# Optimization experiments

Hardware: AMD Instinct MI355X
Metric: run time of the kernel (lower is better)

The kernel has to match this reference:

```python
import jax, jax.numpy as jnp
import numpy as np

N, E = 30000, 180000
IN, H, OUT = 3000, 512, 30


def _segment_softmax(e, dst, n):
    # numerically stable softmax over incoming edges of each destination node
    m = jax.ops.segment_max(e, dst, num_segments=n)
    m = jnp.where(jnp.isfinite(m), m, 0.0)  # nodes with no in-edges
    ex = jnp.exp(e - m[dst])
    den = jax.ops.segment_sum(ex, dst, num_segments=n)
    return ex / den[dst]


def _gat(x, src, dst, Ws, Wd, a_s, a_d, n, alpha=None):
    """edGATConv (heads=1, no self-loops, no bias).
    xs = lin_s(x); attention score from lin_s(x)[src] and lin_d(x)[dst];
    out[i] = sum_{e: dst_e=i} alpha_e * xs[src_e].
    If alpha is given (tie_alpha), reuse it instead of recomputing."""
    xs = x @ Ws.T  # [n, F_out]
    if alpha is None:
        xd = x @ Wd.T
        e = jax.nn.leaky_relu(xs[src] @ a_s + xd[dst] @ a_d, 0.2)  # [E]
        alpha = _segment_softmax(e, dst, n)
    out = jax.ops.segment_sum(alpha[:, None] * xs[src], dst, num_segments=n)
    return out, alpha


def setup_inputs() -> dict:
    key = jax.random.key(0)
    ks = jax.random.split(key, 7)
    features = jax.random.normal(ks[0], (N, IN), dtype=jnp.float32)
    edge_index = jax.random.randint(ks[1], (2, E), 0, N)
    W1s = jax.random.normal(ks[2], (H, IN), dtype=jnp.float32) * 0.02
    W1d = jax.random.normal(ks[3], (H, IN), dtype=jnp.float32) * 0.02
    a1s = jax.random.normal(ks[4], (H,), dtype=jnp.float32) * 0.1
    a1d = jax.random.normal(ks[5], (H,), dtype=jnp.float32) * 0.1
    W2s = jax.random.normal(ks[6], (OUT, H), dtype=jnp.float32) * 0.05
    return {"features": features, "edge_index": edge_index,
            "W1s": W1s, "W1d": W1d, "a1s": a1s, "a1d": a1d, "W2s": W2s}


def reference(features, edge_index, W1s, W1d, a1s, a1d, W2s):
    src, dst = edge_index[0], edge_index[1]
    n = features.shape[0]
    # conv1: attentive GAT layer, stores tie_alpha
    h1, alpha1 = _gat(features, src, dst, W1s, W1d, a1s, a1d, n)
    h1 = jax.nn.elu(h1)
    # conv2: aslinear=True -> plain linear with lin_s
    h2 = h1 @ W2s.T  # [N, OUT]
    # conv3: weights tied to conv2 transposed, alpha tied to conv1
    # W3s = W2s.T so xs3 = h2 @ W3s.T = h2 @ W2s
    h3, _ = _gat(h2, src, dst, W2s.T, None, None, None, n, alpha=alpha1)
    h3 = jax.nn.elu(h3)
    # conv4: aslinear, weight tied to conv1 transposed: h3 @ W4s.T = h3 @ W1s
    h4 = h3 @ W1s  # [N, IN]
    return (h2, h4)
```

## Files before the change

kernel.cpp:

```cpp
#include <hip/hip_runtime.h>

typedef unsigned short u16;
typedef __bf16 bf16_t;
typedef bf16_t bf16x8 __attribute__((ext_vector_type(8)));
typedef float f32x4 __attribute__((ext_vector_type(4)));
typedef u16 u16x8 __attribute__((ext_vector_type(8)));

#define AS1 __attribute__((address_space(1)))
#define AS3 __attribute__((address_space(3)))

__device__ __forceinline__ u16 f2bf(float f) {
    union { float f; unsigned u; } v; v.f = f;
    unsigned r = v.u + 0x7FFFu + ((v.u >> 16) & 1u);
    return (u16)(r >> 16);
}
__device__ __forceinline__ float bf2f(u16 s) {
    union { unsigned u; float f; } v; v.u = ((unsigned)s) << 16;
    return v.f;
}

__device__ __forceinline__ void gload_lds16(const u16* g, u16* l) {
    __builtin_amdgcn_global_load_lds((AS1 const void*)g, (AS3 void*)l, 16, 0, 0);
}

template <bool OUT_BF16, bool GUARD>
__global__ __launch_bounds__(256) void gemm_bt(
    const u16* __restrict__ A, const u16* __restrict__ B, void* __restrict__ Cv,
    int K, int ldc, int Mreal, int Nreal)
{
    __shared__ u16 As[128 * 64];
    __shared__ u16 Bs[128 * 64];
    const int t = threadIdx.x;
    const int w = t >> 6, l = t & 63;

    const int nwg = gridDim.x * gridDim.y;
    const int lin = blockIdx.y * gridDim.x + blockIdx.x;
    const int xcd = lin & 7, loc = lin >> 3;
    const int q = nwg >> 3, r = nwg & 7;
    const int swz = (xcd < r ? xcd * (q + 1) : r * (q + 1) + (xcd - r) * q) + loc;
    const int bx = swz % gridDim.x, by = swz / gridDim.x;

    const int m0 = by * 128, n0 = bx * 128;
    const int wm = (w >> 1) * 64, wn = (w & 1) * 64;

    const int srow = w << 5;
    const int lrow = l >> 3, lc = l & 7;

    f32x4 acc[4][4] = {};

    for (int kt = 0; kt < K; kt += 64) {
#pragma unroll
        for (int i = 0; i < 4; ++i) {
            int row = srow + i * 8 + lrow;
            int gc = ((lc ^ (row & 7)) << 3);
            const u16* ga = A + (size_t)(m0 + row) * K + kt + gc;
            const u16* gb = B + (size_t)(n0 + row) * K + kt + gc;
            u16* la = &As[(srow + i * 8) * 64];
            u16* lb = &Bs[(srow + i * 8) * 64];
            gload_lds16(ga, la);
            gload_lds16(gb, lb);
        }
        asm volatile("s_waitcnt vmcnt(0)");
        __syncthreads();

#pragma unroll
        for (int kk = 0; kk < 2; ++kk) {
            bf16x8 af[4], bfr[4];
            int kc = kk * 4 + (l >> 4);
#pragma unroll
            for (int mi = 0; mi < 4; ++mi) {
                int row = wm + mi * 16 + (l & 15);
                af[mi] = *(const bf16x8*)&As[row * 64 + ((kc ^ (row & 7)) << 3)];
            }
#pragma unroll
            for (int ni = 0; ni < 4; ++ni) {
                int col = wn + ni * 16 + (l & 15);
                bfr[ni] = *(const bf16x8*)&Bs[col * 64 + ((kc ^ (col & 7)) << 3)];
            }
#pragma unroll
            for (int mi = 0; mi < 4; ++mi)
#pragma unroll
                for (int ni = 0; ni < 4; ++ni)
                    acc[mi][ni] = __builtin_amdgcn_mfma_f32_16x16x32_bf16(
                        af[mi], bfr[ni], acc[mi][ni], 0, 0, 0);
        }
        __syncthreads();
    }

#pragma unroll
    for (int mi = 0; mi < 4; ++mi) {
#pragma unroll
        for (int qq = 0; qq < 4; ++qq) {
            int row = m0 + wm + mi * 16 + (l >> 4) * 4 + qq;
            if (GUARD && row >= Mreal) continue;
#pragma unroll
            for (int ni = 0; ni < 4; ++ni) {
                int col = n0 + wn + ni * 16 + (l & 15);
                if (GUARD && col >= Nreal) continue;
                float v = acc[mi][ni][qq];
                if (OUT_BF16) ((u16*)Cv)[(size_t)row * ldc + col] = f2bf(v);
                else          ((float*)Cv)[(size_t)row * ldc + col] = v;
            }
        }
    }
}

__global__ void k_vd(const float* __restrict__ W1d, const float* __restrict__ a1d,
                     float* __restrict__ vd) {
    int i = blockIdx.x * 256 + threadIdx.x;
    if (i >= 3000) return;
    float acc = 0.f;
    for (int h = 0; h < 512; ++h) acc += W1d[(size_t)h * 3000 + i] * a1d[h];
    vd[i] = acc;
}

__global__ void k_w1sb(const float* __restrict__ W1s, u16* __restrict__ wb) {
    int idx = blockIdx.x * 256 + threadIdx.x;
    if (idx >= 512 * 768) return;
    int n = idx / 768, g = idx % 768, k = g * 4;
    ushort4 o = make_ushort4(0, 0, 0, 0);
    if (k < 3000) {
        float4 v = *(const float4*)(W1s + (size_t)n * 3000 + k);
        o.x = f2bf(v.x); o.y = f2bf(v.y); o.z = f2bf(v.z); o.w = f2bf(v.w);
    }
    *(ushort4*)(wb + (size_t)n * 3072 + k) = o;
}

__global__ void k_w1st(const float* __restrict__ W1s, u16* __restrict__ wt) {
    int idx = blockIdx.x * 256 + threadIdx.x;
    if (idx >= 3072 * 512) return;
    int n = idx >> 9, k = idx & 511;
    wt[idx] = (n < 3000) ? f2bf(W1s[(size_t)k * 3000 + n]) : (u16)0;
}

__global__ void k_w2b(const float* __restrict__ W2s, u16* __restrict__ wb) {
    int idx = blockIdx.x * 256 + threadIdx.x;
    if (idx >= 128 * 512) return;
    int n = idx >> 9, k = idx & 511;
    wb[idx] = (n < 30) ? f2bf(W2s[(size_t)n * 512 + k]) : (u16)0;
}

__global__ void k_convX(const float* __restrict__ X, u16* __restrict__ xb,
                        const float* __restrict__ vd, float* __restrict__ sd) {
    __shared__ float red[4];
    int n = blockIdx.x, t = threadIdx.x;
    u16* brow = xb + (size_t)n * 3072;
    if (n < 30000) {
        const float* xrow = X + (size_t)n * 3000;
        float part = 0.f;
#pragma unroll
        for (int it = 0; it < 3; ++it) {
            int c = (t + it * 256) * 4;
            ushort4 o = make_ushort4(0, 0, 0, 0);
            if (c < 3000) {
                float4 v = *(const float4*)(xrow + c);
                float4 wv = *(const float4*)(vd + c);
                o.x = f2bf(v.x); o.y = f2bf(v.y); o.z = f2bf(v.z); o.w = f2bf(v.w);
                part += v.x * wv.x + v.y * wv.y + v.z * wv.z + v.w * wv.w;
            }
            *(ushort4*)(brow + c) = o;
        }
#pragma unroll
        for (int s = 32; s; s >>= 1) part += __shfl_xor(part, s);
        if ((t & 63) == 0) red[t >> 6] = part;
        __syncthreads();
        if (t == 0) sd[n] = red[0] + red[1] + red[2] + red[3];
    } else {
#pragma unroll
        for (int it = 0; it < 3; ++it)
            *(ushort4*)(brow + (t + it * 256) * 4) = make_ushort4(0, 0, 0, 0);
    }
}

__global__ void k_ss(const u16* __restrict__ xs1, const float* __restrict__ a1s,
                     float* __restrict__ ss) {
    int w = threadIdx.x >> 6, l = threadIdx.x & 63;
    int n = blockIdx.x * 4 + w;
    if (n >= 30000) return;
    const u16* row = xs1 + (size_t)n * 512 + l * 8;
    const float* a = a1s + l * 8;
    ushort4 u0 = *(const ushort4*)row;
    ushort4 u1 = *(const ushort4*)(row + 4);
    float4 w0 = *(const float4*)a;
    float4 w1 = *(const float4*)(a + 4);
    float acc = bf2f(u0.x) * w0.x + bf2f(u0.y) * w0.y + bf2f(u0.z) * w0.z + bf2f(u0.w) * w0.w
              + bf2f(u1.x) * w1.x + bf2f(u1.y) * w1.y + bf2f(u1.z) * w1.z + bf2f(u1.w) * w1.w;
#pragma unroll
    for (int s = 32; s; s >>= 1) acc += __shfl_xor(acc, s);
    if (l == 0) ss[n] = acc;
}

__global__ void k_deg(const int* __restrict__ dst, unsigned* __restrict__ deg) {
    int j = blockIdx.x * 256 + threadIdx.x;
    if (j < 180000) atomicAdd(&deg[dst[j]], 1u);
}

__global__ void k_scan1(const unsigned* __restrict__ deg, unsigned* __restrict__ bsum, int n) {
    __shared__ unsigned ws[4];
    int i = blockIdx.x * 256 + threadIdx.x;
    unsigned v = (i < n) ? deg[i] : 0u;
#pragma unroll
    for (int s = 32; s; s >>= 1) v += __shfl_xor(v, s);
    if ((threadIdx.x & 63) == 0) ws[threadIdx.x >> 6] = v;
    __syncthreads();
    if (threadIdx.x == 0) bsum[blockIdx.x] = ws[0] + ws[1] + ws[2] + ws[3];
}

__global__ void k_scan2(const unsigned* __restrict__ bsum, unsigned* __restrict__ boff,
                        unsigned* __restrict__ off_end, int nb) {
    __shared__ unsigned tmp[128];
    int t = threadIdx.x;
    unsigned v = (t < nb) ? bsum[t] : 0u;
    tmp[t] = v;
    __syncthreads();
    for (int s = 1; s < 128; s <<= 1) {
        unsigned a = (t >= s) ? tmp[t - s] : 0u;
        __syncthreads();
        tmp[t] += a;
        __syncthreads();
    }
    if (t < nb) boff[t] = tmp[t] - v;
    if (t == nb - 1) *off_end = tmp[t];
}

__global__ void k_scan3(const unsigned* __restrict__ deg, const unsigned* __restrict__ boff,
                        unsigned* __restrict__ off, unsigned* __restrict__ cur, int n) {
    __shared__ unsigned tmp[256];
    int b = blockIdx.x, t = threadIdx.x, i = b * 256 + t;
    unsigned v = (i < n) ? deg[i] : 0u;
    tmp[t] = v;
    __syncthreads();
    for (int s = 1; s < 256; s <<= 1) {
        unsigned a = (t >= s) ? tmp[t - s] : 0u;
        __syncthreads();
        tmp[t] += a;
        __syncthreads();
    }
    if (i < n) {
        unsigned o = boff[b] + tmp[t] - v;
        off[i] = o;
        cur[i] = o;
    }
}

__global__ void k_fill(const int* __restrict__ dst, unsigned* __restrict__ cur,
                       unsigned* __restrict__ csr) {
    int j = blockIdx.x * 256 + threadIdx.x;
    if (j >= 180000) return;
    unsigned pos = atomicAdd(&cur[dst[j]], 1u);
    csr[pos] = (unsigned)j;
}

__global__ void k_soft(const int* __restrict__ src, const float* __restrict__ ss,
                       const float* __restrict__ sd, float* __restrict__ alpha,
                       const unsigned* __restrict__ csr, const unsigned* __restrict__ off) {
    int t = threadIdx.x;
    int g = t >> 3, l = t & 7;
    int n = blockIdx.x * 32 + g;
    if (n >= 30000) return;
    unsigned lo = off[n], hi = off[n + 1];
    if (lo == hi) return;
    float sdn = sd[n];
    float m = -1e30f;
    for (unsigned i = lo + l; i < hi; i += 8) {
        float v = ss[src[csr[i]]] + sdn;
        v = v > 0.f ? v : 0.2f * v;
        m = fmaxf(m, v);
    }
    m = fmaxf(m, __shfl_xor(m, 1));
    m = fmaxf(m, __shfl_xor(m, 2));
    m = fmaxf(m, __shfl_xor(m, 4));
    float den = 0.f;
    for (unsigned i = lo + l; i < hi; i += 8) {
        float v = ss[src[csr[i]]] + sdn;
        v = v > 0.f ? v : 0.2f * v;
        den += expf(v - m);
    }
    den += __shfl_xor(den, 1);
    den += __shfl_xor(den, 2);
    den += __shfl_xor(den, 4);
    float inv = 1.f / den;
    for (unsigned i = lo + l; i < hi; i += 8) {
        unsigned j = csr[i];
        float v = ss[src[j]] + sdn;
        v = v > 0.f ? v : 0.2f * v;
        alpha[j] = expf(v - m) * inv;
    }
}

__global__ void k_agg(const u16* __restrict__ xin, const float* __restrict__ alpha,
                      const unsigned* __restrict__ csr, const unsigned* __restrict__ off,
                      const int* __restrict__ src, u16* __restrict__ outb, int nvalid) {
    int w = threadIdx.x >> 6, l = threadIdx.x & 63;
    int n = blockIdx.x * 4 + w;
    float acc[8] = {};
    if (n < nvalid) {
        unsigned lo = off[n], hi = off[n + 1];
        for (unsigned i = lo; i < hi; ++i) {
            unsigned j = csr[i];
            float av = alpha[j];
            int sj = src[j];
            u16x8 row = *(const u16x8*)&xin[(size_t)sj * 512 + l * 8];
#pragma unroll
            for (int k = 0; k < 8; ++k) acc[k] += av * bf2f(row[k]);
        }
    }
    u16x8 o;
#pragma unroll
    for (int k = 0; k < 8; ++k) {
        float a = acc[k] > 0.f ? acc[k] : expf(acc[k]) - 1.f;
        o[k] = f2bf(a);
    }
    *(u16x8*)&outb[(size_t)n * 512 + l * 8] = o;
}

__global__ void k_xs3(const float* __restrict__ h2, const float* __restrict__ W2s,
                      u16* __restrict__ xs3) {
    int t = threadIdx.x;
    size_t n0 = (size_t)blockIdx.x * 8;
    float w0[30], w1[30];
#pragma unroll
    for (int o = 0; o < 30; ++o) {
        w0[o] = W2s[(size_t)o * 512 + t];
        w1[o] = W2s[(size_t)o * 512 + t + 256];
    }
    for (int r = 0; r < 8; ++r) {
        size_t n = n0 + r;
        const float* hr = h2 + n * 30;
        float a0 = 0.f, a1 = 0.f;
#pragma unroll
        for (int o = 0; o < 30; ++o) {
            float v = hr[o];
            a0 += v * w0[o];
            a1 += v * w1[o];
        }
        xs3[n * 512 + t] = f2bf(a0);
        xs3[n * 512 + t + 256] = f2bf(a1);
    }
}

extern "C" void kernel_launch(void* const* d_in, const int* in_sizes, int n_in,
                              void* d_out, int out_size, void* d_ws, size_t ws_size,
                              hipStream_t stream) {
    const float* X   = (const float*)d_in[0];
    const int*   ei  = (const int*)d_in[1];
    const float* W1s = (const float*)d_in[2];
    const float* W1d = (const float*)d_in[3];
    const float* a1s = (const float*)d_in[4];
    const float* a1d = (const float*)d_in[5];
    const float* W2s = (const float*)d_in[6];
    const int* src = ei;
    const int* dst = ei + 180000;

    float* out = (float*)d_out;
    float* h2 = out;
    float* h4 = out + 900000;

    char* ob = (char*)(out + 900000);
    u16* xbf  = (u16*)ob;
    u16* xs1b = (u16*)(ob + 184811520);
    u16* h1b  = (u16*)(ob + 184811520 + 30801920);
    u16* xs3b = (u16*)(ob + 184811520 + 30801920 + 30801920);

    char* w = (char*)d_ws;
    auto carve = [&](size_t bytes) { char* p = w; w += (bytes + 255) & ~(size_t)255; return p; };
    u16* w1sb = (u16*)carve((size_t)512 * 3072 * 2);
    u16* w1st = (u16*)carve((size_t)3072 * 512 * 2);
    u16* w2sb = (u16*)carve((size_t)128 * 512 * 2);
    u16* h3b  = (u16*)carve((size_t)30080 * 512 * 2);
    float* vd    = (float*)carve(3000 * 4);
    float* ss    = (float*)carve(30000 * 4);
    float* sd    = (float*)carve(30000 * 4);
    float* alpha = (float*)carve(180000 * 4);
    unsigned* deg = (unsigned*)carve(30000 * 4);
    unsigned* off = (unsigned*)carve(30004 * 4);
    unsigned* cur = (unsigned*)carve(30000 * 4);
    unsigned* csr = (unsigned*)carve(180000 * 4);
    unsigned* bsum = (unsigned*)carve(128 * 4);
    unsigned* boff = (unsigned*)carve(128 * 4);

    hipMemsetAsync(deg, 0, 30000 * 4, stream);

    k_vd  <<<12, 256, 0, stream>>>(W1d, a1d, vd);
    k_w1sb<<<1536, 256, 0, stream>>>(W1s, w1sb);
    k_w1st<<<6144, 256, 0, stream>>>(W1s, w1st);
    k_w2b <<<256, 256, 0, stream>>>(W2s, w2sb);
    k_convX<<<30080, 256, 0, stream>>>(X, xbf, vd, sd);

    gemm_bt<true, false><<<dim3(4, 235), 256, 0, stream>>>(xbf, w1sb, xs1b, 3072, 512, 0, 0);

    k_ss  <<<7500, 256, 0, stream>>>(xs1b, a1s, ss);
    k_deg <<<704, 256, 0, stream>>>(dst, deg);
    k_scan1<<<118, 256, 0, stream>>>(deg, bsum, 30000);
    k_scan2<<<1, 128, 0, stream>>>(bsum, boff, &off[30000], 118);
    k_scan3<<<118, 256, 0, stream>>>(deg, boff, off, cur, 30000);
    k_fill<<<704, 256, 0, stream>>>(dst, cur, csr);
    k_soft<<<938, 256, 0, stream>>>(src, ss, sd, alpha, csr, off);

    k_agg <<<7520, 256, 0, stream>>>(xs1b, alpha, csr, off, src, h1b, 30000);

    gemm_bt<false, true><<<dim3(1, 235), 256, 0, stream>>>(h1b, w2sb, h2, 512, 30, 30000, 30);

    k_xs3 <<<3750, 256, 0, stream>>>(h2, W2s, xs3b);
    k_agg <<<7520, 256, 0, stream>>>(xs3b, alpha, csr, off, src, h3b, 30000);

    gemm_bt<false, true><<<dim3(24, 235), 256, 0, stream>>>(h3b, w1st, h4, 512, 3000, 30000, 3000);
}
```

Baseline: 711.5 us.

## Fold attention source score into input pass and fuse h2/xs3 GEMMs

The source attention score ss is now computed as X·(W1s^T a1s) inside the input-conversion pass, which removes the separate k_ss kernel over xs1. The W2s^T W2s product is precomputed into a combined weight matrix, so one GEMM over h1 writes both h2 and xs3 and the k_xs3 kernel goes away. The W1s transpose kernel is also rewritten to go through an LDS tile for coalesced access. In exchange, the combined GEMM does about five times the N-width of the old h2 GEMM, and ss now comes from fp32 X instead of bf16 xs1, which changes rounding slightly.

```diff
diff --git a/kernel.cpp b/kernel.cpp
--- a/kernel.cpp
+++ b/kernel.cpp
@@ -105,13 +105,95 @@
     }
 }
 
+__global__ __launch_bounds__(256) void gemm_combo(
+    const u16* __restrict__ A, const u16* __restrict__ B,
+    float* __restrict__ h2, u16* __restrict__ xs3)
+{
+    __shared__ u16 As[128 * 64];
+    __shared__ u16 Bs[128 * 64];
+    const int t = threadIdx.x;
+    const int w = t >> 6, l = t & 63;
+
+    const int nwg = gridDim.x * gridDim.y;
+    const int lin = blockIdx.y * gridDim.x + blockIdx.x;
+    const int xcd = lin & 7, loc = lin >> 3;
+    const int q = nwg >> 3, r = nwg & 7;
+    const int swz = (xcd < r ? xcd * (q + 1) : r * (q + 1) + (xcd - r) * q) + loc;
+    const int bx = swz % gridDim.x, by = swz / gridDim.x;
+
+    const int m0 = by * 128, n0 = bx * 128;
+    const int wm = (w >> 1) * 64, wn = (w & 1) * 64;
+    const int srow = w << 5;
+    const int lrow = l >> 3, lc = l & 7;
+
+    f32x4 acc[4][4] = {};
+
+    for (int kt = 0; kt < 512; kt += 64) {
+#pragma unroll
+        for (int i = 0; i < 4; ++i) {
+            int row = srow + i * 8 + lrow;
+            int gc = ((lc ^ (row & 7)) << 3);
+            gload_lds16(A + (size_t)(m0 + row) * 512 + kt + gc, &As[(srow + i * 8) * 64]);
+            gload_lds16(B + (size_t)(n0 + row) * 512 + kt + gc, &Bs[(srow + i * 8) * 64]);
+        }
+        asm volatile("s_waitcnt vmcnt(0)");
+        __syncthreads();
+
+#pragma unroll
+        for (int kk = 0; kk < 2; ++kk) {
+            bf16x8 af[4], bfr[4];
+            int kc = kk * 4 + (l >> 4);
+#pragma unroll
+            for (int mi = 0; mi < 4; ++mi) {
+                int row = wm + mi * 16 + (l & 15);
+                af[mi] = *(const bf16x8*)&As[row * 64 + ((kc ^ (row & 7)) << 3)];
+            }
+#pragma unroll
+            for (int ni = 0; ni < 4; ++ni) {
+                int col = wn + ni * 16 + (l & 15);
+                bfr[ni] = *(const bf16x8*)&Bs[col * 64 + ((kc ^ (col & 7)) << 3)];
+            }
+#pragma unroll
+            for (int mi = 0; mi < 4; ++mi)
+#pragma unroll
+                for (int ni = 0; ni < 4; ++ni)
+                    acc[mi][ni] = __builtin_amdgcn_mfma_f32_16x16x32_bf16(
+                        af[mi], bfr[ni], acc[mi][ni], 0, 0, 0);
+        }
+        __syncthreads();
+    }
+
+#pragma unroll
+    for (int mi = 0; mi < 4; ++mi) {
+#pragma unroll
+        for (int qq = 0; qq < 4; ++qq) {
+            int row = m0 + wm + mi * 16 + (l >> 4) * 4 + qq;
+#pragma unroll
+            for (int ni = 0; ni < 4; ++ni) {
+                int col = n0 + wn + ni * 16 + (l & 15);
+                float v = acc[mi][ni][qq];
+                if (col < 30) {
+                    if (row < 30000) h2[(size_t)row * 30 + col] = v;
+                } else if (col >= 128) {
+                    xs3[(size_t)row * 512 + (col - 128)] = f2bf(v);
+                }
+            }
+        }
+    }
+}
+
 __global__ void k_vd(const float* __restrict__ W1d, const float* __restrict__ a1d,
-                     float* __restrict__ vd) {
+                     const float* __restrict__ W1s, const float* __restrict__ a1s,
+                     float* __restrict__ vd, float* __restrict__ vs) {
     int i = blockIdx.x * 256 + threadIdx.x;
     if (i >= 3000) return;
-    float acc = 0.f;
-    for (int h = 0; h < 512; ++h) acc += W1d[(size_t)h * 3000 + i] * a1d[h];
-    vd[i] = acc;
+    float ad = 0.f, as = 0.f;
+    for (int h = 0; h < 512; ++h) {
+        ad += W1d[(size_t)h * 3000 + i] * a1d[h];
+        as += W1s[(size_t)h * 3000 + i] * a1s[h];
+    }
+    vd[i] = ad;
+    vs[i] = as;
 }
 
 __global__ void k_w1sb(const float* __restrict__ W1s, u16* __restrict__ wb) {
@@ -127,67 +209,79 @@
 }
 
 __global__ void k_w1st(const float* __restrict__ W1s, u16* __restrict__ wt) {
+    __shared__ float tile[64][65];
+    int t = threadIdx.x;
+    int i0 = blockIdx.x * 64;
+    int h0 = blockIdx.y * 64;
+    int il = t & 63, hq = t >> 6;
+#pragma unroll
+    for (int rr = 0; rr < 16; ++rr) {
+        int hl = rr * 4 + hq;
+        int i = i0 + il;
+        tile[hl][il] = (i < 3000) ? W1s[(size_t)(h0 + hl) * 3000 + i] : 0.f;
+    }
+    __syncthreads();
+#pragma unroll
+    for (int rr = 0; rr < 16; ++rr) {
+        int il2 = rr * 4 + hq;
+        wt[(size_t)(i0 + il2) * 512 + h0 + il] = f2bf(tile[il][il2]);
+    }
+}
+
+__global__ void k_wcomb(const float* __restrict__ W2s, u16* __restrict__ wb) {
     int idx = blockIdx.x * 256 + threadIdx.x;
-    if (idx >= 3072 * 512) return;
+    if (idx >= 640 * 512) return;
     int n = idx >> 9, k = idx & 511;
-    wt[idx] = (n < 3000) ? f2bf(W1s[(size_t)k * 3000 + n]) : (u16)0;
-}
-
-__global__ void k_w2b(const float* __restrict__ W2s, u16* __restrict__ wb) {
-    int idx = blockIdx.x * 256 + threadIdx.x;
-    if (idx >= 128 * 512) return;
-    int n = idx >> 9, k = idx & 511;
-    wb[idx] = (n < 30) ? f2bf(W2s[(size_t)n * 512 + k]) : (u16)0;
+    float v = 0.f;
+    if (n < 30) {
+        v = W2s[(size_t)n * 512 + k];
+    } else if (n >= 128) {
+        int i = n - 128;
+        for (int o = 0; o < 30; ++o)
+            v += W2s[(size_t)o * 512 + i] * W2s[(size_t)o * 512 + k];
+    }
+    wb[idx] = f2bf(v);
 }
 
 __global__ void k_convX(const float* __restrict__ X, u16* __restrict__ xb,
-                        const float* __restrict__ vd, float* __restrict__ sd) {
-    __shared__ float red[4];
+                        const float* __restrict__ vd, const float* __restrict__ vs,
+                        float* __restrict__ sd, float* __restrict__ ss) {
+    __shared__ float redd[4], reds[4];
     int n = blockIdx.x, t = threadIdx.x;
     u16* brow = xb + (size_t)n * 3072;
     if (n < 30000) {
         const float* xrow = X + (size_t)n * 3000;
-        float part = 0.f;
+        float pd = 0.f, ps = 0.f;
 #pragma unroll
         for (int it = 0; it < 3; ++it) {
             int c = (t + it * 256) * 4;
             ushort4 o = make_ushort4(0, 0, 0, 0);
             if (c < 3000) {
                 float4 v = *(const float4*)(xrow + c);
-                float4 wv = *(const float4*)(vd + c);
+                float4 wd = *(const float4*)(vd + c);
+                float4 ws = *(const float4*)(vs + c);
                 o.x = f2bf(v.x); o.y = f2bf(v.y); o.z = f2bf(v.z); o.w = f2bf(v.w);
-                part += v.x * wv.x + v.y * wv.y + v.z * wv.z + v.w * wv.w;
+                pd += v.x * wd.x + v.y * wd.y + v.z * wd.z + v.w * wd.w;
+                ps += v.x * ws.x + v.y * ws.y + v.z * ws.z + v.w * ws.w;
             }
             *(ushort4*)(brow + c) = o;
         }
 #pragma unroll
-        for (int s = 32; s; s >>= 1) part += __shfl_xor(part, s);
-        if ((t & 63) == 0) red[t >> 6] = part;
-        __syncthreads();
-        if (t == 0) sd[n] = red[0] + red[1] + red[2] + red[3];
+        for (int s = 32; s; s >>= 1) {
+            pd += __shfl_xor(pd, s);
+            ps += __shfl_xor(ps, s);
+        }
+        if ((t & 63) == 0) { redd[t >> 6] = pd; reds[t >> 6] = ps; }
+        __syncthreads();
+        if (t == 0) {
+            sd[n] = redd[0] + redd[1] + redd[2] + redd[3];
+            ss[n] = reds[0] + reds[1] + reds[2] + reds[3];
+        }
     } else {
 #pragma unroll
         for (int it = 0; it < 3; ++it)
             *(ushort4*)(brow + (t + it * 256) * 4) = make_ushort4(0, 0, 0, 0);
     }
-}
-
-__global__ void k_ss(const u16* __restrict__ xs1, const float* __restrict__ a1s,
-                     float* __restrict__ ss) {
-    int w = threadIdx.x >> 6, l = threadIdx.x & 63;
-    int n = blockIdx.x * 4 + w;
-    if (n >= 30000) return;
-    const u16* row = xs1 + (size_t)n * 512 + l * 8;
-    const float* a = a1s + l * 8;
-    ushort4 u0 = *(const ushort4*)row;
-    ushort4 u1 = *(const ushort4*)(row + 4);
-    float4 w0 = *(const float4*)a;
-    float4 w1 = *(const float4*)(a + 4);
-    float acc = bf2f(u0.x) * w0.x + bf2f(u0.y) * w0.y + bf2f(u0.z) * w0.z + bf2f(u0.w) * w0.w
-              + bf2f(u1.x) * w1.x + bf2f(u1.y) * w1.y + bf2f(u1.z) * w1.z + bf2f(u1.w) * w1.w;
-#pragma unroll
-    for (int s = 32; s; s >>= 1) acc += __shfl_xor(acc, s);
-    if (l == 0) ss[n] = acc;
 }
 
 __global__ void k_deg(const int* __restrict__ dst, unsigned* __restrict__ deg) {
@@ -314,31 +408,6 @@
     *(u16x8*)&outb[(size_t)n * 512 + l * 8] = o;
 }
 
-__global__ void k_xs3(const float* __restrict__ h2, const float* __restrict__ W2s,
-                      u16* __restrict__ xs3) {
-    int t = threadIdx.x;
-    size_t n0 = (size_t)blockIdx.x * 8;
-    float w0[30], w1[30];
-#pragma unroll
-    for (int o = 0; o < 30; ++o) {
-        w0[o] = W2s[(size_t)o * 512 + t];
-        w1[o] = W2s[(size_t)o * 512 + t + 256];
-    }
-    for (int r = 0; r < 8; ++r) {
-        size_t n = n0 + r;
-        const float* hr = h2 + n * 30;
-        float a0 = 0.f, a1 = 0.f;
-#pragma unroll
-        for (int o = 0; o < 30; ++o) {
-            float v = hr[o];
-            a0 += v * w0[o];
-            a1 += v * w1[o];
-        }
-        xs3[n * 512 + t] = f2bf(a0);
-        xs3[n * 512 + t + 256] = f2bf(a1);
-    }
-}
-
 extern "C" void kernel_launch(void* const* d_in, const int* in_sizes, int n_in,
                               void* d_out, int out_size, void* d_ws, size_t ws_size,
                               hipStream_t stream) {
@@ -364,11 +433,12 @@
 
     char* w = (char*)d_ws;
     auto carve = [&](size_t bytes) { char* p = w; w += (bytes + 255) & ~(size_t)255; return p; };
-    u16* w1sb = (u16*)carve((size_t)512 * 3072 * 2);
-    u16* w1st = (u16*)carve((size_t)3072 * 512 * 2);
-    u16* w2sb = (u16*)carve((size_t)128 * 512 * 2);
-    u16* h3b  = (u16*)carve((size_t)30080 * 512 * 2);
-    float* vd    = (float*)carve(3000 * 4);
+    u16* w1sb  = (u16*)carve((size_t)512 * 3072 * 2);
+    u16* w1st  = (u16*)carve((size_t)3072 * 512 * 2);
+    u16* wcomb = (u16*)carve((size_t)640 * 512 * 2);
+    u16* h3b   = (u16*)carve((size_t)30080 * 512 * 2);
+    float* vd    = (float*)carve(3008 * 4);
+    float* vs    = (float*)carve(3008 * 4);
     float* ss    = (float*)carve(30000 * 4);
     float* sd    = (float*)carve(30000 * 4);
     float* alpha = (float*)carve(180000 * 4);
@@ -381,15 +451,14 @@
 
     hipMemsetAsync(deg, 0, 30000 * 4, stream);
 
-    k_vd  <<<12, 256, 0, stream>>>(W1d, a1d, vd);
-    k_w1sb<<<1536, 256, 0, stream>>>(W1s, w1sb);
-    k_w1st<<<6144, 256, 0, stream>>>(W1s, w1st);
-    k_w2b <<<256, 256, 0, stream>>>(W2s, w2sb);
-    k_convX<<<30080, 256, 0, stream>>>(X, xbf, vd, sd);
+    k_vd   <<<12, 256, 0, stream>>>(W1d, a1d, W1s, a1s, vd, vs);
+    k_w1sb <<<1536, 256, 0, stream>>>(W1s, w1sb);
+    k_w1st <<<dim3(48, 8), 256, 0, stream>>>(W1s, w1st);
+    k_wcomb<<<1280, 256, 0, stream>>>(W2s, wcomb);
+    k_convX<<<30080, 256, 0, stream>>>(X, xbf, vd, vs, sd, ss);
 
     gemm_bt<true, false><<<dim3(4, 235), 256, 0, stream>>>(xbf, w1sb, xs1b, 3072, 512, 0, 0);
 
-    k_ss  <<<7500, 256, 0, stream>>>(xs1b, a1s, ss);
     k_deg <<<704, 256, 0, stream>>>(dst, deg);
     k_scan1<<<118, 256, 0, stream>>>(deg, bsum, 30000);
     k_scan2<<<1, 128, 0, stream>>>(bsum, boff, &off[30000], 118);
@@ -399,9 +468,8 @@
 
     k_agg <<<7520, 256, 0, stream>>>(xs1b, alpha, csr, off, src, h1b, 30000);
 
-    gemm_bt<false, true><<<dim3(1, 235), 256, 0, stream>>>(h1b, w2sb, h2, 512, 30, 30000, 30);
-
-    k_xs3 <<<3750, 256, 0, stream>>>(h2, W2s, xs3b);
+    gemm_combo<<<dim3(5, 235), 256, 0, stream>>>(h1b, wcomb, h2, xs3b);
+
     k_agg <<<7520, 256, 0, stream>>>(xs3b, alpha, csr, off, src, h3b, 30000);
 
     gemm_bt<false, true><<<dim3(24, 235), 256, 0, stream>>>(h3b, w1st, h4, 512, 3000, 30000, 3000);
```

New measurement: 724.7 us. Within noise of the previous version (+1.8%).
